# Performance work log

Hardware: AMD Instinct MI355X
Metric: run time of the kernel (lower is better)

Reference implementation:

```python
import jax, jax.numpy as jnp
import numpy as np
from jax import lax

SHIFT_SIZE = 5
PAD = SHIFT_SIZE // 2


def _shift(xn, axis):
    """xn: (B, C, Hp, Wp, Dp) zero-padded volume. Split channels into
    SHIFT_SIZE chunks and roll each chunk by shift in [-PAD, PAD] along `axis`."""
    chunks = jnp.split(xn, SHIFT_SIZE, axis=1)
    shifted = [jnp.roll(c, s, axis=axis) for c, s in zip(chunks, range(-PAD, PAD + 1))]
    return jnp.concatenate(shifted, axis=1)


def _shift_tokens(x, H, W, D, axis):
    """x: (B, N, C) tokens -> shifted tokens (B, N, C). axis=2 shifts H, axis=3 shifts W."""
    B, N, C = x.shape
    xn = x.transpose(0, 2, 1).reshape(B, C, H, W, D)
    xn = jnp.pad(xn, ((0, 0), (0, 0), (PAD, PAD), (PAD, PAD), (PAD, PAD)))
    xs = _shift(xn, axis)
    xs = xs[:, :, PAD:PAD + H, PAD:PAD + W, PAD:PAD + D]
    return xs.reshape(B, C, N).transpose(0, 2, 1)


def setup_inputs() -> dict:
    key = jax.random.key(0)
    ks = jax.random.split(key, 4)
    B, H, W, D = 2, 32, 32, 32
    N = H * W * D
    Cin, Ch = 160, 640
    return {
        "x": jax.random.normal(ks[0], (B, N, Cin), jnp.float32),
        "fc1_w": jax.random.normal(ks[1], (Ch, Cin), jnp.float32) * 0.02,
        "fc1_b": jnp.zeros((Ch,), jnp.float32),
        "dw_w": jax.random.normal(ks[2], (Ch, 1, 3, 3, 3), jnp.float32) * (2.0 / 27.0) ** 0.5,
        "dw_b": jnp.zeros((Ch,), jnp.float32),
        "fc2_w": jax.random.normal(ks[3], (Cin, Ch), jnp.float32) * 0.02,
        "fc2_b": jnp.zeros((Cin,), jnp.float32),
        "H": H, "W": W, "D": D,
    }


def reference(x, fc1_w, fc1_b, dw_w, dw_b, fc2_w, fc2_b, H, W, D):
    B, N, Cin = x.shape
    Ch = fc1_w.shape[0]
    # shift block 1: roll along H (axis 2)
    xs = _shift_tokens(x, H, W, D, axis=2)
    # fc1
    h = jnp.einsum('bnc,hc->bnh', xs, fc1_w) + fc1_b  # (B, N, Ch)
    # depthwise 3x3x3 conv
    hv = h.transpose(0, 2, 1).reshape(B, Ch, H, W, D)
    hv = lax.conv_general_dilated(
        hv, dw_w, window_strides=(1, 1, 1), padding='SAME',
        feature_group_count=Ch,
        dimension_numbers=('NCDHW', 'OIDHW', 'NCDHW'))
    hv = hv + dw_b[None, :, None, None, None]
    hv = jax.nn.gelu(hv, approximate=False)
    h = hv.reshape(B, Ch, N).transpose(0, 2, 1)
    # shift block 2: roll along W (axis 3)
    hs = _shift_tokens(h, H, W, D, axis=3)
    # fc2
    out = jnp.einsum('bnh,oh->bno', hs, fc2_w) + fc2_b  # (B, N, Cin)
    return out
```

## Files before the change

kernel.cpp:

```cpp
#include <hip/hip_runtime.h>
#include <hip/hip_bf16.h>
#include <math.h>

#define DEVI __device__ __forceinline__

typedef _Float16 f16;
typedef f16 f16x2 __attribute__((ext_vector_type(2)));
typedef f16 f16x4 __attribute__((ext_vector_type(4)));
typedef f16 f16x8 __attribute__((ext_vector_type(8)));
typedef float f32x4 __attribute__((ext_vector_type(4)));

constexpr int Bb = 2, Hh = 32, Ww = 32, Dd = 32;
constexpr int Nn = Hh * Ww * Dd;
constexpr int BN = Bb * Nn;
constexpr int CIN = 160, CHH = 640;
constexpr int PD = 34;
constexpr int PT = PD * PD * PD;

constexpr size_t W1_OFF  = 0;
constexpr size_t W2_OFF  = W1_OFF + (size_t)CHH * CIN * 2;
constexpr size_t WTH_OFF = W2_OFF + (size_t)CIN * CHH * 2;
constexpr size_t ZP_OFF  = WTH_OFF + 34816;
constexpr size_t U_OFF   = 458752;
constexpr size_t H1P_OFF = U_OFF + (size_t)BN * CHH * 2;

DEVI void async16(const void* g, void* l) {
  __builtin_amdgcn_global_load_lds(
      (const __attribute__((address_space(1))) void*)g,
      (__attribute__((address_space(3))) void*)l, 16, 0, 0);
}

__global__ __launch_bounds__(256) void k_prep_w(const float* __restrict__ fc1w,
                                                const float* __restrict__ fc2w,
                                                const float* __restrict__ dww,
                                                f16* __restrict__ w1h,
                                                f16* __restrict__ w2h,
                                                f16* __restrict__ wTh,
                                                unsigned* __restrict__ zp) {
  int i = blockIdx.x * 256 + threadIdx.x;
  const int NW = CHH * CIN;
  if (i < NW) {
    w1h[i] = (f16)fc1w[i];
  } else if (i < 2 * NW) {
    int j = i - NW;
    w2h[j] = (f16)fc2w[j];
  } else if (i < 2 * NW + 27 * CHH) {
    int j = i - 2 * NW;
    int ch = j / 27, tap = j % 27;
    wTh[tap * CHH + ch] = (f16)dww[j];
  } else if (i < 2 * NW + 27 * CHH + 2048) {
    zp[i - (2 * NW + 27 * CHH)] = 0u;
  }
}

__global__ __launch_bounds__(256) void k_zero_pad(f16* __restrict__ h1p) {
  int g = blockIdx.x * 256 + threadIdx.x;
  int p = g / 80;
  int c = g - p * 80;
  if (p >= 2 * PT) return;
  int r = p % PT;
  int hp = r / (PD * PD);
  int r2 = r % (PD * PD);
  int wp = r2 / PD, dp = r2 % PD;
  bool pad = (hp == 0) | (hp == PD - 1) | (wp == 0) | (wp == PD - 1) |
             (dp == 0) | (dp == PD - 1);
  if (!pad) return;
  f16x8 z = {};
  *(f16x8*)&h1p[(size_t)p * CHH + c * 8] = z;
}

__global__ __launch_bounds__(256) void k_gemm1(const float* __restrict__ x,
                                               const f16* __restrict__ w1h,
                                               const float* __restrict__ fc1b,
                                               f16* __restrict__ h1p) {
  constexpr int LDA = 168;
  __shared__ f16 lsA[128 * LDA];
  __shared__ f16 lsB[128 * 32];
  const int tid = threadIdx.x;
  const int lane = tid & 63, wave = tid >> 6;
  const int row0 = blockIdx.x * 128;
  const int wr = wave >> 1, wc = wave & 1;
  const int rl = lane & 15, kb = (lane >> 4) * 8;

#pragma unroll
  for (int i = 0; i < 20; ++i) {
    int c = i * 256 + tid;
    int row = c / 40;
    int q = c - row * 40;
    int ch0 = q * 4;
    int ks = ch0 >> 5;
    int s = ks - 2;
    int t = row0 + row;
    int h = (t >> 10) & 31;
    int hs = h - s;
    float4 v = {0.f, 0.f, 0.f, 0.f};
    if (hs >= 0 && hs < 32)
      v = *(const float4*)&x[(long)(t - s * 1024) * CIN + ch0];
    f16x4 o4;
    o4[0] = (f16)v.x; o4[1] = (f16)v.y; o4[2] = (f16)v.z; o4[3] = (f16)v.w;
    *(f16x4*)&lsA[row * LDA + ch0] = o4;
  }
  __syncthreads();

  for (int nt = 0; nt < 5; ++nt) {
    const int col0 = nt * 128;
    f32x4 acc[4][4] = {};
    for (int ks = 0; ks < 5; ++ks) {
#pragma unroll
      for (int issue = 0; issue < 2; ++issue) {
        int c = issue * 256 + tid;
        int br = c >> 2;
        int kc = (c & 3) * 8;
        const f16* src = w1h + (size_t)(col0 + br) * CIN + ks * 32 + kc;
        async16(src, (char*)lsB + issue * 4096 + wave * 1024);
      }
      __syncthreads();
      f16x8 af[4], bfr[4];
#pragma unroll
      for (int mi = 0; mi < 4; ++mi)
        af[mi] = *(const f16x8*)&lsA[(wr * 64 + mi * 16 + rl) * LDA + ks * 32 + kb];
#pragma unroll
      for (int ni = 0; ni < 4; ++ni)
        bfr[ni] = *(const f16x8*)&lsB[(wc * 64 + ni * 16 + rl) * 32 + kb];
#pragma unroll
      for (int mi = 0; mi < 4; ++mi)
#pragma unroll
        for (int ni = 0; ni < 4; ++ni)
          acc[mi][ni] = __builtin_amdgcn_mfma_f32_16x16x32_f16(af[mi], bfr[ni], acc[mi][ni], 0, 0, 0);
      __syncthreads();
    }
    const int rq = lane >> 4;
#pragma unroll
    for (int mi = 0; mi < 4; ++mi) {
      int rowq = row0 + wr * 64 + mi * 16 + rq * 4;
      int bq = rowq >> 15;
      int nq = rowq & 32767;
      int hq = nq >> 10, wq = (nq >> 5) & 31, dq = nq & 31;
      size_t pos = (size_t)((bq * PD + hq + 1) * PD + (wq + 1)) * PD + (dq + 1);
      f16* dst0 = h1p + pos * CHH;
#pragma unroll
      for (int ni = 0; ni < 4; ++ni) {
        int col = col0 + wc * 64 + ni * 16 + rl;
        float bias = fc1b[col];
#pragma unroll
        for (int r = 0; r < 4; ++r)
          dst0[(size_t)r * CHH + col] = (f16)(acc[mi][ni][r] + bias);
      }
    }
  }
}

__global__ __launch_bounds__(256) void k_conv(const f16* __restrict__ h1p,
                                              const f16* __restrict__ wTh,
                                              const float* __restrict__ dwb,
                                              f16* __restrict__ h2h) {
  __shared__ f16 lw[27 * 64];
  __shared__ f16 lb[64];
  const int tid = threadIdx.x;
  const int cg = blockIdx.y;
#pragma unroll
  for (int i = 0; i < 7; ++i) {
    int idx = i * 256 + tid;
    if (idx < 27 * 64) lw[idx] = wTh[(idx >> 6) * CHH + cg * 64 + (idx & 63)];
  }
  if (tid < 64) lb[tid] = (f16)dwb[cg * 64 + tid];
  __syncthreads();

  const int lane = tid & 63, wave = tid >> 6;
  const int line = blockIdx.x * 4 + wave;
  const int c8 = lane & 7, dq = lane >> 3;
  const int d0 = dq * 4;
  const int ch0 = cg * 64 + c8 * 8;
  const int w = line & 31, h = (line >> 5) & 31, b = line >> 10;

  const size_t cidx = (size_t)((b * PD + h) * PD + w) * PD + d0;
  const f16* base = h1p + cidx * CHH + ch0;

  f16x8 acc[4];
  {
    f16x8 binit = *(const f16x8*)&lb[c8 * 8];
    acc[0] = binit; acc[1] = binit; acc[2] = binit; acc[3] = binit;
  }

#pragma unroll
  for (int kz = 0; kz < 3; ++kz) {
#pragma unroll
    for (int ky = 0; ky < 3; ++ky) {
      const f16* pb = base + (size_t)(kz * PD + ky) * PD * CHH;
      f16x8 wt[3];
#pragma unroll
      for (int kx = 0; kx < 3; ++kx)
        wt[kx] = *(const f16x8*)&lw[((kz * 9 + ky * 3 + kx) << 6) + c8 * 8];
      f16x8 v[6];
#pragma unroll
      for (int j = 0; j < 6; ++j)
        v[j] = *(const f16x8*)(pb + (size_t)j * CHH);
#pragma unroll
      for (int o = 0; o < 4; ++o)
#pragma unroll
        for (int kx = 0; kx < 3; ++kx)
          acc[o] = v[o + kx] * wt[kx] + acc[o];
    }
  }

  const ptrdiff_t obase = (ptrdiff_t)(line * 32 + d0) * CHH + ch0;
#pragma unroll
  for (int o = 0; o < 4; ++o) {
    f16x8 xa = acc[o];
    f16x8 ov;
#pragma unroll
    for (int j = 0; j < 8; j += 2) {
      float g01[2];
#pragma unroll
      for (int u2 = 0; u2 < 2; ++u2) {
        float xv = (float)xa[j + u2];
        float x2 = xv * xv;
        float uu = xv * (2.3022078f + 0.102943324f * x2);
        float e = __builtin_exp2f(uu);
        float r = __builtin_amdgcn_rcpf(1.0f + e);
        g01[u2] = xv - xv * r;
      }
      f16x2 pk = __builtin_bit_cast(f16x2, __builtin_amdgcn_cvt_pkrtz(g01[0], g01[1]));
      ov[j] = pk[0]; ov[j + 1] = pk[1];
    }
    *(f16x8*)&h2h[obase + (ptrdiff_t)o * CHH] = ov;
  }
}

__global__ __launch_bounds__(256) void k_gemm2(const f16* __restrict__ h2h,
                                               const f16* __restrict__ w2h,
                                               const float* __restrict__ fc2b,
                                               const f16* __restrict__ zp,
                                               float* __restrict__ out) {
  __shared__ f16 lsA[128 * 64];
  __shared__ f16 lsB[160 * 64];
  const int tid = threadIdx.x, lane = tid & 63, wave = tid >> 6;
  const int row0 = blockIdx.x * 128;
  const int rl = lane & 15, kb = (lane >> 4) * 8;

  f32x4 acc[2][10] = {};

  for (int kt = 0; kt < 10; ++kt) {
    __syncthreads();
    const int k0 = kt * 64;
    const int s = (k0 >> 7) - 2;
#pragma unroll
    for (int issue = 0; issue < 4; ++issue) {
      int c = issue * 256 + tid;
      int ar = c >> 3;
      int kc = (c & 7) * 8;
      int t = row0 + ar;
      int w = (t >> 5) & 31;
      int wsv = w - s;
      const f16* src;
      if (wsv >= 0 && wsv < 32)
        src = h2h + (size_t)(t - s * 32) * CHH + k0 + kc;
      else
        src = zp + (size_t)(c & 63) * 8;
      async16(src, (char*)lsA + issue * 4096 + wave * 1024);
    }
#pragma unroll
    for (int issue = 0; issue < 5; ++issue) {
      int c = issue * 256 + tid;
      int br = c >> 3;
      int kc = (c & 7) * 8;
      const f16* src = w2h + (size_t)br * CHH + k0 + kc;
      async16(src, (char*)lsB + issue * 4096 + wave * 1024);
    }
    __syncthreads();
#pragma unroll
    for (int kk = 0; kk < 2; ++kk) {
      f16x8 af[2], bfr[10];
#pragma unroll
      for (int mi = 0; mi < 2; ++mi)
        af[mi] = *(const f16x8*)&lsA[(wave * 32 + mi * 16 + rl) * 64 + kk * 32 + kb];
#pragma unroll
      for (int ni = 0; ni < 10; ++ni)
        bfr[ni] = *(const f16x8*)&lsB[(ni * 16 + rl) * 64 + kk * 32 + kb];
#pragma unroll
      for (int mi = 0; mi < 2; ++mi)
#pragma unroll
        for (int ni = 0; ni < 10; ++ni)
          acc[mi][ni] = __builtin_amdgcn_mfma_f32_16x16x32_f16(af[mi], bfr[ni], acc[mi][ni], 0, 0, 0);
    }
  }
  const int rq = lane >> 4;
#pragma unroll
  for (int mi = 0; mi < 2; ++mi) {
#pragma unroll
    for (int ni = 0; ni < 10; ++ni) {
      int col = ni * 16 + rl;
      float bias = fc2b[col];
#pragma unroll
      for (int r = 0; r < 4; ++r) {
        int row = row0 + wave * 32 + mi * 16 + rq * 4 + r;
        out[(size_t)row * CIN + col] = acc[mi][ni][r] + bias;
      }
    }
  }
}

extern "C" void kernel_launch(void* const* d_in, const int* in_sizes, int n_in,
                              void* d_out, int out_size, void* d_ws, size_t ws_size,
                              hipStream_t stream) {
  const float* x    = (const float*)d_in[0];
  const float* fc1w = (const float*)d_in[1];
  const float* fc1b = (const float*)d_in[2];
  const float* dww  = (const float*)d_in[3];
  const float* dwb  = (const float*)d_in[4];
  const float* fc2w = (const float*)d_in[5];
  const float* fc2b = (const float*)d_in[6];

  char* ws = (char*)d_ws;
  f16* w1h  = (f16*)(ws + W1_OFF);
  f16* w2h  = (f16*)(ws + W2_OFF);
  f16* wTh  = (f16*)(ws + WTH_OFF);
  f16* zp   = (f16*)(ws + ZP_OFF);
  f16* h2h  = (f16*)(ws + U_OFF);
  f16* h1p  = (f16*)(ws + H1P_OFF);
  float* out = (float*)d_out;

  k_zero_pad<<<(2 * PT * 80) / 256, 256, 0, stream>>>(h1p);
  k_prep_w<<<876, 256, 0, stream>>>(fc1w, fc2w, dww, w1h, w2h, wTh, (unsigned*)zp);
  k_gemm1<<<512, 256, 0, stream>>>(x, w1h, fc1b, h1p);
  dim3 gc(BN / 32 / 4, 10);
  k_conv<<<gc, 256, 0, stream>>>(h1p, wTh, dwb, h2h);
  k_gemm2<<<512, 256, 0, stream>>>(h2h, w2h, fc2b, zp, out);
}
```

Before: 141.5 us.

## Swizzle GEMM LDS tiles, merge prep kernels, remap conv blocks across XCDs

Adds an XOR swizzle to the LDS layouts of the B tile in gemm1 and both A and B tiles in gemm2, to cut bank conflicts on the f16x8 MFMA operand reads. Merges the weight-prep and pad-zeroing kernels into one launch to save launch overhead. Flattens the conv grid and remaps block IDs so that consecutive blocks on each XCD work on neighbouring spatial lines, which should improve L2 reuse of halo data. The swizzle must match between the async-load addresses and the fragment-read addresses, so a mismatch there would silently corrupt results.

```diff
diff --git a/kernel.cpp b/kernel.cpp
--- a/kernel.cpp
+++ b/kernel.cpp
@@ -30,31 +30,36 @@
       (__attribute__((address_space(3))) void*)l, 16, 0, 0);
 }
 
-__global__ __launch_bounds__(256) void k_prep_w(const float* __restrict__ fc1w,
-                                                const float* __restrict__ fc2w,
-                                                const float* __restrict__ dww,
-                                                f16* __restrict__ w1h,
-                                                f16* __restrict__ w2h,
-                                                f16* __restrict__ wTh,
-                                                unsigned* __restrict__ zp) {
-  int i = blockIdx.x * 256 + threadIdx.x;
-  const int NW = CHH * CIN;
-  if (i < NW) {
-    w1h[i] = (f16)fc1w[i];
-  } else if (i < 2 * NW) {
-    int j = i - NW;
-    w2h[j] = (f16)fc2w[j];
-  } else if (i < 2 * NW + 27 * CHH) {
-    int j = i - 2 * NW;
-    int ch = j / 27, tap = j % 27;
-    wTh[tap * CHH + ch] = (f16)dww[j];
-  } else if (i < 2 * NW + 27 * CHH + 2048) {
-    zp[i - (2 * NW + 27 * CHH)] = 0u;
-  }
-}
-
-__global__ __launch_bounds__(256) void k_zero_pad(f16* __restrict__ h1p) {
-  int g = blockIdx.x * 256 + threadIdx.x;
+constexpr int PREPW_BLOCKS = 876;
+constexpr int ZPAD_BLOCKS  = (2 * PT * 80 + 255) / 256;
+
+__global__ __launch_bounds__(256) void k_prep(const float* __restrict__ fc1w,
+                                              const float* __restrict__ fc2w,
+                                              const float* __restrict__ dww,
+                                              f16* __restrict__ w1h,
+                                              f16* __restrict__ w2h,
+                                              f16* __restrict__ wTh,
+                                              unsigned* __restrict__ zp,
+                                              f16* __restrict__ h1p) {
+  const int bid = blockIdx.x;
+  const int tid = threadIdx.x;
+  if (bid < PREPW_BLOCKS) {
+    int i = bid * 256 + tid;
+    const int NW = CHH * CIN;
+    if (i < NW) {
+      w1h[i] = (f16)fc1w[i];
+    } else if (i < 2 * NW) {
+      w2h[i - NW] = (f16)fc2w[i - NW];
+    } else if (i < 2 * NW + 27 * CHH) {
+      int j = i - 2 * NW;
+      int ch = j / 27, tap = j % 27;
+      wTh[tap * CHH + ch] = (f16)dww[j];
+    } else if (i < 2 * NW + 27 * CHH + 2048) {
+      zp[i - (2 * NW + 27 * CHH)] = 0u;
+    }
+    return;
+  }
+  int g = (bid - PREPW_BLOCKS) * 256 + tid;
   int p = g / 80;
   int c = g - p * 80;
   if (p >= 2 * PT) return;
@@ -110,8 +115,8 @@
       for (int issue = 0; issue < 2; ++issue) {
         int c = issue * 256 + tid;
         int br = c >> 2;
-        int kc = (c & 3) * 8;
-        const f16* src = w1h + (size_t)(col0 + br) * CIN + ks * 32 + kc;
+        int ju = (c & 3) ^ (br & 3);
+        const f16* src = w1h + (size_t)(col0 + br) * CIN + ks * 32 + ju * 8;
         async16(src, (char*)lsB + issue * 4096 + wave * 1024);
       }
       __syncthreads();
@@ -120,8 +125,11 @@
       for (int mi = 0; mi < 4; ++mi)
         af[mi] = *(const f16x8*)&lsA[(wr * 64 + mi * 16 + rl) * LDA + ks * 32 + kb];
 #pragma unroll
-      for (int ni = 0; ni < 4; ++ni)
-        bfr[ni] = *(const f16x8*)&lsB[(wc * 64 + ni * 16 + rl) * 32 + kb];
+      for (int ni = 0; ni < 4; ++ni) {
+        int row = wc * 64 + ni * 16 + rl;
+        int u = (lane >> 4) ^ (rl & 3);
+        bfr[ni] = *(const f16x8*)&lsB[row * 32 + u * 8];
+      }
 #pragma unroll
       for (int mi = 0; mi < 4; ++mi)
 #pragma unroll
@@ -157,7 +165,10 @@
   __shared__ f16 lw[27 * 64];
   __shared__ f16 lb[64];
   const int tid = threadIdx.x;
-  const int cg = blockIdx.y;
+  const int bid = blockIdx.x;
+  const int wg = (bid & 7) * 640 + (bid >> 3);
+  const int cg = wg % 10;
+  const int quad = wg / 10;
 #pragma unroll
   for (int i = 0; i < 7; ++i) {
     int idx = i * 256 + tid;
@@ -167,7 +178,7 @@
   __syncthreads();
 
   const int lane = tid & 63, wave = tid >> 6;
-  const int line = blockIdx.x * 4 + wave;
+  const int line = quad * 4 + wave;
   const int c8 = lane & 7, dq = lane >> 3;
   const int d0 = dq * 4;
   const int ch0 = cg * 64 + c8 * 8;
@@ -236,19 +247,20 @@
   __shared__ f16 lsB[160 * 64];
   const int tid = threadIdx.x, lane = tid & 63, wave = tid >> 6;
   const int row0 = blockIdx.x * 128;
-  const int rl = lane & 15, kb = (lane >> 4) * 8;
+  const int rl = lane & 15;
 
   f32x4 acc[2][10] = {};
 
   for (int kt = 0; kt < 10; ++kt) {
     __syncthreads();
     const int k0 = kt * 64;
-    const int s = (k0 >> 7) - 2;
+    const int s = (kt >> 1) - 2;
 #pragma unroll
     for (int issue = 0; issue < 4; ++issue) {
       int c = issue * 256 + tid;
       int ar = c >> 3;
-      int kc = (c & 7) * 8;
+      int ju = (c & 7) ^ (ar & 7);
+      int kc = ju * 8;
       int t = row0 + ar;
       int w = (t >> 5) & 31;
       int wsv = w - s;
@@ -263,8 +275,8 @@
     for (int issue = 0; issue < 5; ++issue) {
       int c = issue * 256 + tid;
       int br = c >> 3;
-      int kc = (c & 7) * 8;
-      const f16* src = w2h + (size_t)br * CHH + k0 + kc;
+      int ju = (c & 7) ^ (br & 7);
+      const f16* src = w2h + (size_t)br * CHH + k0 + ju * 8;
       async16(src, (char*)lsB + issue * 4096 + wave * 1024);
     }
     __syncthreads();
@@ -272,11 +284,17 @@
     for (int kk = 0; kk < 2; ++kk) {
       f16x8 af[2], bfr[10];
 #pragma unroll
-      for (int mi = 0; mi < 2; ++mi)
-        af[mi] = *(const f16x8*)&lsA[(wave * 32 + mi * 16 + rl) * 64 + kk * 32 + kb];
-#pragma unroll
-      for (int ni = 0; ni < 10; ++ni)
-        bfr[ni] = *(const f16x8*)&lsB[(ni * 16 + rl) * 64 + kk * 32 + kb];
+      for (int mi = 0; mi < 2; ++mi) {
+        int row = wave * 32 + mi * 16 + rl;
+        int u = (kk * 4 + (lane >> 4)) ^ (rl & 7);
+        af[mi] = *(const f16x8*)&lsA[row * 64 + u * 8];
+      }
+#pragma unroll
+      for (int ni = 0; ni < 10; ++ni) {
+        int row = ni * 16 + rl;
+        int u = (kk * 4 + (lane >> 4)) ^ (rl & 7);
+        bfr[ni] = *(const f16x8*)&lsB[row * 64 + u * 8];
+      }
 #pragma unroll
       for (int mi = 0; mi < 2; ++mi)
 #pragma unroll
@@ -320,10 +338,9 @@
   f16* h1p  = (f16*)(ws + H1P_OFF);
   float* out = (float*)d_out;
 
-  k_zero_pad<<<(2 * PT * 80) / 256, 256, 0, stream>>>(h1p);
-  k_prep_w<<<876, 256, 0, stream>>>(fc1w, fc2w, dww, w1h, w2h, wTh, (unsigned*)zp);
+  k_prep<<<PREPW_BLOCKS + ZPAD_BLOCKS, 256, 0, stream>>>(
+      fc1w, fc2w, dww, w1h, w2h, wTh, (unsigned*)zp, h1p);
   k_gemm1<<<512, 256, 0, stream>>>(x, w1h, fc1b, h1p);
-  dim3 gc(BN / 32 / 4, 10);
-  k_conv<<<gc, 256, 0, stream>>>(h1p, wTh, dwb, h2h);
+  k_conv<<<5120, 256, 0, stream>>>(h1p, wTh, dwb, h2h);
   k_gemm2<<<512, 256, 0, stream>>>(h2h, w2h, fc2b, zp, out);
 }
```

Result: faster. 131.0 us (-7.5%).
